# Performance work log

Hardware: AMD Instinct MI355X
Metric: run time of the kernel (lower is better)

The kernel has to match this reference:

```python
import jax, jax.numpy as jnp
import numpy as np
import math

B, T, D, H, L = 8, 1024, 128, 8, 2
DH = D // H            # head dim = 16
F = 2 * D              # ffn hidden = 256 (FFN_EXPANSION=2)
SCALE = math.sqrt(DH)  # sqrt of Q last dim per head


def layernorm(x, g, b):
    m = jnp.mean(x, axis=-1, keepdims=True)
    v = jnp.var(x, axis=-1, keepdims=True)
    return (x - m) * jax.lax.rsqrt(v + 1e-5) * g + b


def setup_inputs() -> dict:
    key = jax.random.key(0)
    ks = jax.random.split(key, 16)
    s = 1.0 / math.sqrt(D)
    r = lambda i, shp: jax.random.normal(ks[i], shp, dtype=jnp.float32) * s
    return {
        "x": jax.random.normal(ks[0], (B, T, D), dtype=jnp.float32),
        "y": jax.random.normal(ks[1], (B, T, D), dtype=jnp.float32),
        # shared qkv projections (no bias), per layer
        "Wq": r(2, (L, D, D)), "Wk": r(3, (L, D, D)), "Wv": r(4, (L, D, D)),
        "Wox": r(5, (L, D, D)), "box": jnp.zeros((L, D), jnp.float32),
        "Woy": r(6, (L, D, D)), "boy": jnp.zeros((L, D), jnp.float32),
        "ln1x_g": jnp.ones((L, D), jnp.float32), "ln1x_b": jnp.zeros((L, D), jnp.float32),
        "ln1y_g": jnp.ones((L, D), jnp.float32), "ln1y_b": jnp.zeros((L, D), jnp.float32),
        "ln2x_g": jnp.ones((L, D), jnp.float32), "ln2x_b": jnp.zeros((L, D), jnp.float32),
        "ln2y_g": jnp.ones((L, D), jnp.float32), "ln2y_b": jnp.zeros((L, D), jnp.float32),
        "fx_w1": r(7, (L, D, F)), "fx_b1": jnp.zeros((L, F), jnp.float32),
        "fx_w2": r(8, (L, F, D)), "fx_b2": jnp.zeros((L, D), jnp.float32),
        "fy_w1": r(9, (L, D, F)), "fy_b1": jnp.zeros((L, F), jnp.float32),
        "fy_w2": r(10, (L, F, D)), "fy_b2": jnp.zeros((L, D), jnp.float32),
    }


def _heads(t):
    # (B,T,D) -> (B,T,H,DH)
    return t.reshape(B, T, H, DH)


def _block(x, y, Wq, Wk, Wv, Wox, box, Woy, boy,
           ln1x_g, ln1x_b, ln1y_g, ln1y_b, ln2x_g, ln2x_b, ln2y_g, ln2y_b,
           fx_w1, fx_b1, fx_w2, fx_b2, fy_w1, fy_b1, fy_w2, fy_b2):
    xn = layernorm(x, ln1x_g, ln1x_b)
    yn = layernorm(y, ln1y_g, ln1y_b)
    # x-branch: Q from y, K/V from x ; y-branch: Q from x, K/V from y
    qx = _heads(yn @ Wq); kx = _heads(xn @ Wk); vx = _heads(xn @ Wv)
    qy = _heads(xn @ Wq); ky = _heads(yn @ Wk); vy = _heads(yn @ Wv)
    ax = jnp.einsum('bthd,bshd->bhts', qx, kx)  # (B,H,T,T)
    ay = jnp.einsum('bthd,bshd->bhts', qy, ky)
    # cat over heads + reshape(B,2,H,T,T) + mean(dim=1) == per-head average
    w = jax.nn.softmax((ax + ay) * (0.5 / SCALE), axis=-1)
    o1 = jnp.einsum('bhts,bshd->bthd', w, vx).reshape(B, T, D) @ Wox + box
    o2 = jnp.einsum('bhts,bshd->bthd', w, vy).reshape(B, T, D) @ Woy + boy
    x = x + o1
    y = y + o2
    xn2 = layernorm(x, ln2x_g, ln2x_b)
    yn2 = layernorm(y, ln2y_g, ln2y_b)
    x = x + jax.nn.gelu(xn2 @ fx_w1 + fx_b1, approximate=False) @ fx_w2 + fx_b2
    y = y + jax.nn.gelu(yn2 @ fy_w1 + fy_b1, approximate=False) @ fy_w2 + fy_b2
    return x, y


def reference(x, y, Wq, Wk, Wv, Wox, box, Woy, boy,
              ln1x_g, ln1x_b, ln1y_g, ln1y_b, ln2x_g, ln2x_b, ln2y_g, ln2y_b,
              fx_w1, fx_b1, fx_w2, fx_b2, fy_w1, fy_b1, fy_w2, fy_b2):
    for i in range(L):
        x, y = _block(x, y, Wq[i], Wk[i], Wv[i], Wox[i], box[i], Woy[i], boy[i],
                      ln1x_g[i], ln1x_b[i], ln1y_g[i], ln1y_b[i],
                      ln2x_g[i], ln2x_b[i], ln2y_g[i], ln2y_b[i],
                      fx_w1[i], fx_b1[i], fx_w2[i], fx_b2[i],
                      fy_w1[i], fy_b1[i], fy_w2[i], fy_b2[i])
    return (x, y)
```

## Files before the change

kernel.cpp:

```cpp
#include <hip/hip_runtime.h>
#include <cstddef>

#define BB   8
#define TT   1024
#define DDIM 128
#define HH   8
#define DHH  16
#define FF   256
#define BT   (BB * TT)

typedef unsigned short u16;
typedef __attribute__((ext_vector_type(8))) short short8;
typedef __attribute__((ext_vector_type(4))) float f32x4;

__device__ __forceinline__ u16 bf(float x) {
  unsigned u = __builtin_bit_cast(unsigned, x);
  u += 0x7fffu + ((u >> 16) & 1u);
  return (u16)(u >> 16);
}
__device__ __forceinline__ u16 bft(float x) {
  return (u16)(__builtin_bit_cast(unsigned, x) >> 16);
}
__device__ __forceinline__ float gelu_f(float x) {
  const float t = x * (0.79788456f + 0.03567740814f * x * x);
  return x / (1.0f + __expf(-2.0f * t));
}

struct PrepP { const float* W; u16* Wt; int K; int N; };
struct PrepArgs { PrepP p[18]; };

__global__ __launch_bounds__(256) void prep_k(PrepArgs a) {
  const PrepP pp = a.p[blockIdx.z];
  const int n0 = blockIdx.x * 64, k0 = blockIdx.y * 64;
  if (n0 >= pp.N || k0 >= pp.K) return;
  __shared__ float tile[64][65];
  const int tid = threadIdx.x;
  #pragma unroll
  for (int t = tid; t < 1024; t += 256) {
    const int kk = t >> 4, nn4 = (t & 15) << 2;
    float4 v = *(const float4*)(pp.W + (size_t)(k0 + kk) * pp.N + n0 + nn4);
    tile[nn4 + 0][kk] = v.x; tile[nn4 + 1][kk] = v.y;
    tile[nn4 + 2][kk] = v.z; tile[nn4 + 3][kk] = v.w;
  }
  __syncthreads();
  #pragma unroll
  for (int t = tid; t < 1024; t += 256) {
    const int nn = t >> 4, kk4 = (t & 15) << 2;
    ushort4 o;
    o.x = bf(tile[nn][kk4 + 0]); o.y = bf(tile[nn][kk4 + 1]);
    o.z = bf(tile[nn][kk4 + 2]); o.w = bf(tile[nn][kk4 + 3]);
    *(ushort4*)(pp.Wt + (size_t)(n0 + nn) * pp.K + k0 + kk4) = o;
  }
}

__global__ __launch_bounds__(256) void ln0_k(const float* __restrict__ X,
                                             const float* __restrict__ Y,
                                             const float* __restrict__ gx,
                                             const float* __restrict__ bx,
                                             const float* __restrict__ gy,
                                             const float* __restrict__ by,
                                             u16* __restrict__ ox,
                                             u16* __restrict__ oy) {
  const int which = blockIdx.y;
  const float* in = which ? Y : X;
  const float* g  = which ? gy : gx;
  const float* b  = which ? by : bx;
  u16* out        = which ? oy : ox;
  const int row  = blockIdx.x * 4 + (threadIdx.x >> 6);
  const int lane = threadIdx.x & 63;

  float2 v = *(const float2*)(in + (size_t)row * DDIM + lane * 2);
  float s  = v.x + v.y;
  float sq = v.x * v.x + v.y * v.y;
  #pragma unroll
  for (int off = 32; off >= 1; off >>= 1) {
    s  += __shfl_xor(s, off);
    sq += __shfl_xor(sq, off);
  }
  const float mean = s * (1.0f / DDIM);
  const float var  = sq * (1.0f / DDIM) - mean * mean;
  const float r    = rsqrtf(var + 1e-5f);
  float2 gg = *(const float2*)(g + lane * 2);
  float2 bb = *(const float2*)(b + lane * 2);
  ushort2 o;
  o.x = bf((v.x - mean) * r * gg.x + bb.x);
  o.y = bf((v.y - mean) * r * gg.y + bb.y);
  *(ushort2*)(out + (size_t)row * DDIM + lane * 2) = o;
}

struct GemmP { const u16* A; const u16* Wt; const float* bias; const float* res;
               float* outF; u16* outB; const float* g; const float* b; };
struct GemmArgs { GemmP p[6]; int ln; };

__global__ __launch_bounds__(256) void gemmf_k(GemmArgs a) {
  const GemmP pp = a.p[blockIdx.z];
  const int m0 = blockIdx.y * 32;
  __shared__ __align__(16) u16 As[32][136];
  __shared__ __align__(16) u16 Bs[128][136];
  __shared__ float2 stats[32][2];
  const int tid  = threadIdx.x;
  const int w    = tid >> 6;
  const int lane = tid & 63;
  const int l15  = lane & 15;
  const int quad = lane >> 4;
  const int wr = w & 1, wc = w >> 1;

  f32x4 acc[4];
  #pragma unroll
  for (int j = 0; j < 4; ++j) acc[j] = {0.f, 0.f, 0.f, 0.f};

  #pragma unroll
  for (int t = tid; t < 512; t += 256) {
    const int r = t >> 4, g8 = (t & 15) << 3;
    *(short8*)&As[r][g8] = *(const short8*)(pp.A + (size_t)(m0 + r) * 128 + g8);
  }
  #pragma unroll
  for (int t = tid; t < 2048; t += 256) {
    const int r = t >> 4, g8 = (t & 15) << 3;
    *(short8*)&Bs[r][g8] = *(const short8*)(pp.Wt + (size_t)r * 128 + g8);
  }
  __syncthreads();
  #pragma unroll
  for (int ks = 0; ks < 4; ++ks) {
    const short8 ar = *(const short8*)&As[wr * 16 + l15][ks * 32 + quad * 8];
    #pragma unroll
    for (int j = 0; j < 4; ++j) {
      const short8 br = *(const short8*)&Bs[wc * 64 + j * 16 + l15][ks * 32 + quad * 8];
      acc[j] = __builtin_amdgcn_mfma_f32_16x16x32_bf16(ar, br, acc[j], 0, 0, 0);
    }
  }

  #pragma unroll
  for (int j = 0; j < 4; ++j) {
    const int n = wc * 64 + j * 16 + l15;
    const float bias_v = pp.bias ? pp.bias[n] : 0.f;
    #pragma unroll
    for (int reg = 0; reg < 4; ++reg) {
      const int m = m0 + wr * 16 + quad * 4 + reg;
      float v = acc[j][reg] + bias_v;
      if (pp.res) v += pp.res[(size_t)m * 128 + n];
      acc[j][reg] = v;
      if (pp.outF) pp.outF[(size_t)m * 128 + n] = v;
    }
  }

  if (!a.ln) {
    #pragma unroll
    for (int j = 0; j < 4; ++j) {
      const int n = wc * 64 + j * 16 + l15;
      #pragma unroll
      for (int reg = 0; reg < 4; ++reg) {
        const int m = m0 + wr * 16 + quad * 4 + reg;
        pp.outB[(size_t)m * 128 + n] = bf(acc[j][reg]);
      }
    }
    return;
  }

  #pragma unroll
  for (int reg = 0; reg < 4; ++reg) {
    float s = 0.f, q = 0.f;
    #pragma unroll
    for (int j = 0; j < 4; ++j) { const float v = acc[j][reg]; s += v; q += v * v; }
    #pragma unroll
    for (int off = 8; off >= 1; off >>= 1) {
      s += __shfl_xor(s, off, 16);
      q += __shfl_xor(q, off, 16);
    }
    if (l15 == 0) stats[wr * 16 + quad * 4 + reg][wc] = make_float2(s, q);
  }
  __syncthreads();
  #pragma unroll
  for (int reg = 0; reg < 4; ++reg) {
    const int mloc = wr * 16 + quad * 4 + reg;
    const float2 s0 = stats[mloc][0], s1 = stats[mloc][1];
    const float mean = (s0.x + s1.x) * (1.0f / 128.f);
    const float var  = (s0.y + s1.y) * (1.0f / 128.f) - mean * mean;
    const float r    = rsqrtf(var + 1e-5f);
    #pragma unroll
    for (int j = 0; j < 4; ++j) {
      const int n = wc * 64 + j * 16 + l15;
      pp.outB[(size_t)(m0 + mloc) * 128 + n] =
          bf((acc[j][reg] - mean) * r * pp.g[n] + pp.b[n]);
    }
  }
}

struct FfnP { const u16* A; const u16* W1t; const float* b1;
              const u16* W2t; const float* b2; const float* res;
              float* outF; u16* outB; const float* g; const float* b; };
struct FfnArgs { FfnP p[2]; int ln; };

__global__ __launch_bounds__(256) void ffn_k(FfnArgs a) {
  const FfnP pp = a.p[blockIdx.y];
  const int m0 = blockIdx.x * 32;
  __shared__ __align__(16) u16 As[32][136];
  __shared__ __align__(16) u16 Bs[128][136];
  __shared__ __align__(16) u16 Hs[32][264];
  __shared__ float2 stats[32][2];
  const int tid  = threadIdx.x;
  const int w    = tid >> 6;
  const int lane = tid & 63;
  const int l15  = lane & 15;
  const int quad = lane >> 4;
  const int wr = w & 1, wc = w >> 1;

  #pragma unroll
  for (int t = tid; t < 512; t += 256) {
    const int r = t >> 4, g8 = (t & 15) << 3;
    *(short8*)&As[r][g8] = *(const short8*)(pp.A + (size_t)(m0 + r) * 128 + g8);
  }

  for (int nh = 0; nh < 2; ++nh) {
    #pragma unroll
    for (int t = tid; t < 2048; t += 256) {
      const int r = t >> 4, g8 = (t & 15) << 3;
      *(short8*)&Bs[r][g8] = *(const short8*)(pp.W1t + (size_t)(nh * 128 + r) * 128 + g8);
    }
    __syncthreads();
    f32x4 acc[4];
    #pragma unroll
    for (int j = 0; j < 4; ++j) acc[j] = {0.f, 0.f, 0.f, 0.f};
    #pragma unroll
    for (int ks = 0; ks < 4; ++ks) {
      const short8 ar = *(const short8*)&As[wr * 16 + l15][ks * 32 + quad * 8];
      #pragma unroll
      for (int j = 0; j < 4; ++j) {
        const short8 br = *(const short8*)&Bs[wc * 64 + j * 16 + l15][ks * 32 + quad * 8];
        acc[j] = __builtin_amdgcn_mfma_f32_16x16x32_bf16(ar, br, acc[j], 0, 0, 0);
      }
    }
    #pragma unroll
    for (int j = 0; j < 4; ++j) {
      const int n = wc * 64 + j * 16 + l15;
      const float bias_v = pp.b1[nh * 128 + n];
      #pragma unroll
      for (int reg = 0; reg < 4; ++reg) {
        const int mloc = wr * 16 + quad * 4 + reg;
        Hs[mloc][nh * 128 + n] = bf(gelu_f(acc[j][reg] + bias_v));
      }
    }
    __syncthreads();
  }

  f32x4 acc2[4];
  #pragma unroll
  for (int j = 0; j < 4; ++j) acc2[j] = {0.f, 0.f, 0.f, 0.f};
  for (int kh = 0; kh < 2; ++kh) {
    #pragma unroll
    for (int t = tid; t < 2048; t += 256) {
      const int r = t >> 4, g8 = (t & 15) << 3;
      *(short8*)&Bs[r][g8] = *(const short8*)(pp.W2t + (size_t)r * 256 + kh * 128 + g8);
    }
    __syncthreads();
    #pragma unroll
    for (int ks = 0; ks < 4; ++ks) {
      const short8 ar = *(const short8*)&Hs[wr * 16 + l15][kh * 128 + ks * 32 + quad * 8];
      #pragma unroll
      for (int j = 0; j < 4; ++j) {
        const short8 br = *(const short8*)&Bs[wc * 64 + j * 16 + l15][ks * 32 + quad * 8];
        acc2[j] = __builtin_amdgcn_mfma_f32_16x16x32_bf16(ar, br, acc2[j], 0, 0, 0);
      }
    }
    __syncthreads();
  }

  #pragma unroll
  for (int j = 0; j < 4; ++j) {
    const int n = wc * 64 + j * 16 + l15;
    const float bias_v = pp.b2[n];
    #pragma unroll
    for (int reg = 0; reg < 4; ++reg) {
      const int m = m0 + wr * 16 + quad * 4 + reg;
      float v = acc2[j][reg] + bias_v + pp.res[(size_t)m * 128 + n];
      acc2[j][reg] = v;
      pp.outF[(size_t)m * 128 + n] = v;
    }
  }
  if (!a.ln) return;
  #pragma unroll
  for (int reg = 0; reg < 4; ++reg) {
    float s = 0.f, q = 0.f;
    #pragma unroll
    for (int j = 0; j < 4; ++j) { const float v = acc2[j][reg]; s += v; q += v * v; }
    #pragma unroll
    for (int off = 8; off >= 1; off >>= 1) {
      s += __shfl_xor(s, off, 16);
      q += __shfl_xor(q, off, 16);
    }
    if (l15 == 0) stats[wr * 16 + quad * 4 + reg][wc] = make_float2(s, q);
  }
  __syncthreads();
  #pragma unroll
  for (int reg = 0; reg < 4; ++reg) {
    const int mloc = wr * 16 + quad * 4 + reg;
    const float2 s0 = stats[mloc][0], s1 = stats[mloc][1];
    const float mean = (s0.x + s1.x) * (1.0f / 128.f);
    const float var  = (s0.y + s1.y) * (1.0f / 128.f) - mean * mean;
    const float r    = rsqrtf(var + 1e-5f);
    #pragma unroll
    for (int j = 0; j < 4; ++j) {
      const int n = wc * 64 + j * 16 + l15;
      pp.outB[(size_t)(m0 + mloc) * 128 + n] =
          bf((acc2[j][reg] - mean) * r * pp.g[n] + pp.b[n]);
    }
  }
}

__global__ __launch_bounds__(256) void attn_k(const u16* __restrict__ qx,
                                              const u16* __restrict__ kx,
                                              const u16* __restrict__ vx,
                                              const u16* __restrict__ qy,
                                              const u16* __restrict__ ky,
                                              const u16* __restrict__ vy,
                                              u16* __restrict__ o1,
                                              u16* __restrict__ o2) {
  const int t0 = blockIdx.x * 64;
  const int bh = blockIdx.y;
  const int b = bh >> 3, h = bh & 7;
  const size_t base = (size_t)b * TT * DDIM + h * DHH;

  __shared__ __align__(16) u16 Ks[2][128][40];
  __shared__ __align__(16) u16 Vt[2][32][136];
  __shared__ __align__(16) u16 Ps[64][136];

  const int tid  = threadIdx.x;
  const int w    = tid >> 6;
  const int lane = tid & 63;
  const int l15  = lane & 15;
  const int quad = lane >> 4;

  const u16* qp = (quad < 2) ? qx : qy;
  const int dq = (quad & 1) * 8;
  const short8 qa = *(const short8*)(qp + base + (size_t)(t0 + w * 16 + l15) * DDIM + dq);

  f32x4 Of0 = {0.f, 0.f, 0.f, 0.f};
  f32x4 Of1 = {0.f, 0.f, 0.f, 0.f};
  float l_i[4] = {0.f, 0.f, 0.f, 0.f};

  const int ks_s = tid >> 2, ks_c = tid & 3;
  const u16* ks_p = (ks_c < 2) ? kx : ky;
  const int ks_d8 = (ks_c & 1) * 8;
  const int ks_col = (ks_c < 2 ? 0 : 16) + ks_d8;

  const u16* vs_p = (w < 2) ? vx : vy;
  const int vs_cc = (w & 1) * 8;
  const int vs_cb = (w < 2 ? 0 : 16) + vs_cc;

  #define STAGE(kt, buf)                                                          \
    do {                                                                          \
      const int s0_ = (kt) * 128;                                                 \
      _Pragma("unroll")                                                           \
      for (int p = 0; p < 2; ++p) {                                               \
        const int s = ks_s + p * 64;                                              \
        *(short8*)&Ks[buf][s][ks_col] =                                           \
            *(const short8*)(ks_p + base + (size_t)(s0_ + s) * DDIM + ks_d8);     \
      }                                                                           \
      _Pragma("unroll")                                                           \
      for (int p = 0; p < 2; ++p) {                                               \
        const int sl = lane + p * 64;                                             \
        const short8 v8 =                                                         \
            *(const short8*)(vs_p + base + (size_t)(s0_ + sl) * DDIM + vs_cc);    \
        _Pragma("unroll")                                                         \
        for (int e = 0; e < 8; ++e) Vt[buf][vs_cb + e][sl] = (u16)v8[e];          \
      }                                                                           \
    } while (0)

  STAGE(0, 0);

  for (int kt = 0; kt < TT / 128; ++kt) {
    const int buf = kt & 1;
    __syncthreads();
    if (kt + 1 < TT / 128) STAGE(kt + 1, buf ^ 1);

    f32x4 Sf[8];
    #pragma unroll
    for (int t = 0; t < 8; ++t) {
      short8 kb = *(const short8*)&Ks[buf][t * 16 + l15][quad * 8];
      f32x4 z = {0.f, 0.f, 0.f, 0.f};
      Sf[t] = __builtin_amdgcn_mfma_f32_16x16x32_bf16(qa, kb, z, 0, 0, 0);
    }

    #pragma unroll
    for (int reg = 0; reg < 4; ++reg) {
      const int q = w * 16 + quad * 4 + reg;
      float sum = 0.f;
      #pragma unroll
      for (int t = 0; t < 8; ++t) {
        const float p = exp2f(Sf[t][reg] * 0.18033688011112042f);
        sum += p;
        Ps[q][t * 16 + l15] = bft(p);
      }
      l_i[reg] += sum;
    }

    #pragma unroll
    for (int sh = 0; sh < 4; ++sh) {
      short8 pa  = *(const short8*)&Ps[w * 16 + l15][sh * 32 + quad * 8];
      short8 vb0 = *(const short8*)&Vt[buf][l15][sh * 32 + quad * 8];
      short8 vb1 = *(const short8*)&Vt[buf][16 + l15][sh * 32 + quad * 8];
      Of0 = __builtin_amdgcn_mfma_f32_16x16x32_bf16(pa, vb0, Of0, 0, 0, 0);
      Of1 = __builtin_amdgcn_mfma_f32_16x16x32_bf16(pa, vb1, Of1, 0, 0, 0);
    }
  }
  #undef STAGE

  #pragma unroll
  for (int reg = 0; reg < 4; ++reg) {
    float l = l_i[reg];
    #pragma unroll
    for (int off = 8; off >= 1; off >>= 1) l += __shfl_xor(l, off, 16);
    const float inv = 1.0f / l;
    const size_t r = base + (size_t)(t0 + w * 16 + quad * 4 + reg) * DDIM + l15;
    o1[r] = bf(Of0[reg] * inv);
    o2[r] = bf(Of1[reg] * inv);
  }
}

extern "C" void kernel_launch(void* const* d_in, const int* in_sizes, int n_in,
                              void* d_out, int out_size, void* d_ws, size_t ws_size,
                              hipStream_t stream) {
  const float* x_in  = (const float*)d_in[0];
  const float* y_in  = (const float*)d_in[1];
  const float* Wq    = (const float*)d_in[2];
  const float* Wk    = (const float*)d_in[3];
  const float* Wv    = (const float*)d_in[4];
  const float* Wox   = (const float*)d_in[5];
  const float* box   = (const float*)d_in[6];
  const float* Woy   = (const float*)d_in[7];
  const float* boy   = (const float*)d_in[8];
  const float* ln1xg = (const float*)d_in[9];
  const float* ln1xb = (const float*)d_in[10];
  const float* ln1yg = (const float*)d_in[11];
  const float* ln1yb = (const float*)d_in[12];
  const float* ln2xg = (const float*)d_in[13];
  const float* ln2xb = (const float*)d_in[14];
  const float* ln2yg = (const float*)d_in[15];
  const float* ln2yb = (const float*)d_in[16];
  const float* fxw1  = (const float*)d_in[17];
  const float* fxb1  = (const float*)d_in[18];
  const float* fxw2  = (const float*)d_in[19];
  const float* fxb2  = (const float*)d_in[20];
  const float* fyw1  = (const float*)d_in[21];
  const float* fyb1  = (const float*)d_in[22];
  const float* fyw2  = (const float*)d_in[23];
  const float* fyb2  = (const float*)d_in[24];

  const size_t S = (size_t)BT * DDIM;
  float* X = (float*)d_out;
  float* Y = X + S;

  char* wsb = (char*)d_ws;
  auto carve = [&](size_t bytes) { char* p = wsb; wsb += (bytes + 255) & ~(size_t)255; return p; };
  u16* xn  = (u16*)carve(S * 2);
  u16* yn  = (u16*)carve(S * 2);
  u16* qx  = (u16*)carve(S * 2);
  u16* kx  = (u16*)carve(S * 2);
  u16* vx  = (u16*)carve(S * 2);
  u16* qy  = (u16*)carve(S * 2);
  u16* ky  = (u16*)carve(S * 2);
  u16* vy  = (u16*)carve(S * 2);
  u16* ob1 = (u16*)carve(S * 2);
  u16* ob2 = (u16*)carve(S * 2);
  u16* WqT[2], *WkT[2], *WvT[2], *WoxT[2], *WoyT[2];
  u16* f1xT[2], *f1yT[2], *f2xT[2], *f2yT[2];
  for (int l = 0; l < 2; ++l) {
    WqT[l]  = (u16*)carve(16384 * 2);
    WkT[l]  = (u16*)carve(16384 * 2);
    WvT[l]  = (u16*)carve(16384 * 2);
    WoxT[l] = (u16*)carve(16384 * 2);
    WoyT[l] = (u16*)carve(16384 * 2);
    f1xT[l] = (u16*)carve(32768 * 2);
    f1yT[l] = (u16*)carve(32768 * 2);
    f2xT[l] = (u16*)carve(32768 * 2);
    f2yT[l] = (u16*)carve(32768 * 2);
  }

  {
    PrepArgs a;
    int idx = 0;
    for (int l = 0; l < 2; ++l) {
      a.p[idx++] = {Wq  + (size_t)l * 16384, WqT[l],  128, 128};
      a.p[idx++] = {Wk  + (size_t)l * 16384, WkT[l],  128, 128};
      a.p[idx++] = {Wv  + (size_t)l * 16384, WvT[l],  128, 128};
      a.p[idx++] = {Wox + (size_t)l * 16384, WoxT[l], 128, 128};
      a.p[idx++] = {Woy + (size_t)l * 16384, WoyT[l], 128, 128};
      a.p[idx++] = {fxw1 + (size_t)l * 32768, f1xT[l], 128, 256};
      a.p[idx++] = {fyw1 + (size_t)l * 32768, f1yT[l], 128, 256};
      a.p[idx++] = {fxw2 + (size_t)l * 32768, f2xT[l], 256, 128};
      a.p[idx++] = {fyw2 + (size_t)l * 32768, f2yT[l], 256, 128};
    }
    prep_k<<<dim3(4, 4, 18), 256, 0, stream>>>(a);
  }

  ln0_k<<<dim3(BT / 4, 2), 256, 0, stream>>>(x_in, y_in, ln1xg, ln1xb, ln1yg, ln1yb, xn, yn);

  for (int l = 0; l < 2; ++l) {
    const size_t bo  = (size_t)l * DDIM;
    const size_t fbo = (size_t)l * FF;

    {
      GemmArgs a = {}; a.ln = 0;
      a.p[0] = {yn, WqT[l], nullptr, nullptr, nullptr, qx, nullptr, nullptr};
      a.p[1] = {xn, WkT[l], nullptr, nullptr, nullptr, kx, nullptr, nullptr};
      a.p[2] = {xn, WvT[l], nullptr, nullptr, nullptr, vx, nullptr, nullptr};
      a.p[3] = {xn, WqT[l], nullptr, nullptr, nullptr, qy, nullptr, nullptr};
      a.p[4] = {yn, WkT[l], nullptr, nullptr, nullptr, ky, nullptr, nullptr};
      a.p[5] = {yn, WvT[l], nullptr, nullptr, nullptr, vy, nullptr, nullptr};
      gemmf_k<<<dim3(1, BT / 32, 6), 256, 0, stream>>>(a);
    }
    attn_k<<<dim3(TT / 64, BB * HH), 256, 0, stream>>>(qx, kx, vx, qy, ky, vy, ob1, ob2);
    {
      const float* resx = (l == 0) ? x_in : X;
      const float* resy = (l == 0) ? y_in : Y;
      GemmArgs a = {}; a.ln = 1;
      a.p[0] = {ob1, WoxT[l], box + bo, resx, X, xn, ln2xg + bo, ln2xb + bo};
      a.p[1] = {ob2, WoyT[l], boy + bo, resy, Y, yn, ln2yg + bo, ln2yb + bo};
      gemmf_k<<<dim3(1, BT / 32, 2), 256, 0, stream>>>(a);
    }
    {
      FfnArgs a = {}; a.ln = (l == 0) ? 1 : 0;
      if (l == 0) {
        a.p[0] = {xn, f1xT[l], fxb1 + fbo, f2xT[l], fxb2 + bo, X, X, xn,
                  ln1xg + DDIM, ln1xb + DDIM};
        a.p[1] = {yn, f1yT[l], fyb1 + fbo, f2yT[l], fyb2 + bo, Y, Y, yn,
                  ln1yg + DDIM, ln1yb + DDIM};
      } else {
        a.p[0] = {xn, f1xT[l], fxb1 + fbo, f2xT[l], fxb2 + bo, X, X, nullptr,
                  nullptr, nullptr};
        a.p[1] = {yn, f1yT[l], fyb1 + fbo, f2yT[l], fyb2 + bo, Y, Y, nullptr,
                  nullptr, nullptr};
      }
      ffn_k<<<dim3(BT / 32, 2), 256, 0, stream>>>(a);
    }
  }
}
```

Measured before the change: 270.9 us.

## Write V pre-transposed from projection GEMM and shrink attention key tiles

The QKV projection GEMM now writes V directly in a head-major transposed layout (b,h,d,s), so the attention kernel can stage V with vectorized short8 loads instead of scattering elements into a transposed shared tile. The attention kernel also switches to 64-key tiles with smaller shared buffers, and swaps the MFMA operand order so each lane holds scores for one query row. That allows packed ushort4 stores of P and a single row-sum reduction per lane. The trade-off is twice as many loop iterations and barriers per block, plus strided 8-byte transposed stores in the GEMM epilogue.

```diff
diff --git a/kernel.cpp b/kernel.cpp
--- a/kernel.cpp
+++ b/kernel.cpp
@@ -89,7 +89,7 @@
 }
 
 struct GemmP { const u16* A; const u16* Wt; const float* bias; const float* res;
-               float* outF; u16* outB; const float* g; const float* b; };
+               float* outF; u16* outB; const float* g; const float* b; u16* outT; };
 struct GemmArgs { GemmP p[6]; int ln; };
 
 __global__ __launch_bounds__(256) void gemmf_k(GemmArgs a) {
@@ -130,6 +130,21 @@
     }
   }
 
+  if (pp.outT) {
+    const int m_base = m0 + wr * 16 + quad * 4;
+    const int bb_ = m_base >> 10, s = m_base & 1023;
+    #pragma unroll
+    for (int j = 0; j < 4; ++j) {
+      const int n = wc * 64 + j * 16 + l15;
+      const int h = n >> 4, c = n & 15;
+      ushort4 o;
+      o.x = bf(acc[j][0]); o.y = bf(acc[j][1]);
+      o.z = bf(acc[j][2]); o.w = bf(acc[j][3]);
+      *(ushort4*)(pp.outT + (((size_t)(bb_ * 8 + h) * 16 + c) << 10) + s) = o;
+    }
+    return;
+  }
+
   #pragma unroll
   for (int j = 0; j < 4; ++j) {
     const int n = wc * 64 + j * 16 + l15;
@@ -145,13 +160,15 @@
   }
 
   if (!a.ln) {
-    #pragma unroll
-    for (int j = 0; j < 4; ++j) {
-      const int n = wc * 64 + j * 16 + l15;
+    if (pp.outB) {
       #pragma unroll
-      for (int reg = 0; reg < 4; ++reg) {
-        const int m = m0 + wr * 16 + quad * 4 + reg;
-        pp.outB[(size_t)m * 128 + n] = bf(acc[j][reg]);
+      for (int j = 0; j < 4; ++j) {
+        const int n = wc * 64 + j * 16 + l15;
+        #pragma unroll
+        for (int reg = 0; reg < 4; ++reg) {
+          const int m = m0 + wr * 16 + quad * 4 + reg;
+          pp.outB[(size_t)m * 128 + n] = bf(acc[j][reg]);
+        }
       }
     }
     return;
@@ -309,10 +326,10 @@
 
 __global__ __launch_bounds__(256) void attn_k(const u16* __restrict__ qx,
                                               const u16* __restrict__ kx,
-                                              const u16* __restrict__ vx,
                                               const u16* __restrict__ qy,
                                               const u16* __restrict__ ky,
-                                              const u16* __restrict__ vy,
+                                              const u16* __restrict__ vtx,
+                                              const u16* __restrict__ vty,
                                               u16* __restrict__ o1,
                                               u16* __restrict__ o2) {
   const int t0 = blockIdx.x * 64;
@@ -320,9 +337,9 @@
   const int b = bh >> 3, h = bh & 7;
   const size_t base = (size_t)b * TT * DDIM + h * DHH;
 
-  __shared__ __align__(16) u16 Ks[2][128][40];
-  __shared__ __align__(16) u16 Vt[2][32][136];
-  __shared__ __align__(16) u16 Ps[64][136];
+  __shared__ __align__(16) u16 Ks[2][64][40];
+  __shared__ __align__(16) u16 Vt[2][32][72];
+  __shared__ __align__(16) u16 Ps[64][72];
 
   const int tid  = threadIdx.x;
   const int w    = tid >> 6;
@@ -336,66 +353,55 @@
 
   f32x4 Of0 = {0.f, 0.f, 0.f, 0.f};
   f32x4 Of1 = {0.f, 0.f, 0.f, 0.f};
-  float l_i[4] = {0.f, 0.f, 0.f, 0.f};
+  float l_i = 0.f;
 
   const int ks_s = tid >> 2, ks_c = tid & 3;
   const u16* ks_p = (ks_c < 2) ? kx : ky;
   const int ks_d8 = (ks_c & 1) * 8;
   const int ks_col = (ks_c < 2 ? 0 : 16) + ks_d8;
 
-  const u16* vs_p = (w < 2) ? vx : vy;
-  const int vs_cc = (w & 1) * 8;
-  const int vs_cb = (w < 2 ? 0 : 16) + vs_cc;
+  const int vs_c = tid >> 3;
+  const int vs_s8 = (tid & 7) * 8;
+  const u16* vs_row = (vs_c < 16) ? (vtx + (((size_t)bh * 16 + vs_c) << 10))
+                                  : (vty + (((size_t)bh * 16 + (vs_c - 16)) << 10));
 
   #define STAGE(kt, buf)                                                          \
     do {                                                                          \
-      const int s0_ = (kt) * 128;                                                 \
-      _Pragma("unroll")                                                           \
-      for (int p = 0; p < 2; ++p) {                                               \
-        const int s = ks_s + p * 64;                                              \
-        *(short8*)&Ks[buf][s][ks_col] =                                           \
-            *(const short8*)(ks_p + base + (size_t)(s0_ + s) * DDIM + ks_d8);     \
-      }                                                                           \
-      _Pragma("unroll")                                                           \
-      for (int p = 0; p < 2; ++p) {                                               \
-        const int sl = lane + p * 64;                                             \
-        const short8 v8 =                                                         \
-            *(const short8*)(vs_p + base + (size_t)(s0_ + sl) * DDIM + vs_cc);    \
-        _Pragma("unroll")                                                         \
-        for (int e = 0; e < 8; ++e) Vt[buf][vs_cb + e][sl] = (u16)v8[e];          \
-      }                                                                           \
+      const int s0_ = (kt) * 64;                                                  \
+      *(short8*)&Ks[buf][ks_s][ks_col] =                                          \
+          *(const short8*)(ks_p + base + (size_t)(s0_ + ks_s) * DDIM + ks_d8);    \
+      *(short8*)&Vt[buf][vs_c][vs_s8] = *(const short8*)(vs_row + s0_ + vs_s8);   \
     } while (0)
 
   STAGE(0, 0);
 
-  for (int kt = 0; kt < TT / 128; ++kt) {
+  for (int kt = 0; kt < TT / 64; ++kt) {
     const int buf = kt & 1;
     __syncthreads();
-    if (kt + 1 < TT / 128) STAGE(kt + 1, buf ^ 1);
-
-    f32x4 Sf[8];
-    #pragma unroll
-    for (int t = 0; t < 8; ++t) {
+    if (kt + 1 < TT / 64) STAGE(kt + 1, buf ^ 1);
+
+    f32x4 Sf[4];
+    #pragma unroll
+    for (int t = 0; t < 4; ++t) {
       short8 kb = *(const short8*)&Ks[buf][t * 16 + l15][quad * 8];
       f32x4 z = {0.f, 0.f, 0.f, 0.f};
-      Sf[t] = __builtin_amdgcn_mfma_f32_16x16x32_bf16(qa, kb, z, 0, 0, 0);
-    }
-
-    #pragma unroll
-    for (int reg = 0; reg < 4; ++reg) {
-      const int q = w * 16 + quad * 4 + reg;
-      float sum = 0.f;
-      #pragma unroll
-      for (int t = 0; t < 8; ++t) {
-        const float p = exp2f(Sf[t][reg] * 0.18033688011112042f);
-        sum += p;
-        Ps[q][t * 16 + l15] = bft(p);
-      }
-      l_i[reg] += sum;
-    }
-
-    #pragma unroll
-    for (int sh = 0; sh < 4; ++sh) {
+      Sf[t] = __builtin_amdgcn_mfma_f32_16x16x32_bf16(kb, qa, z, 0, 0, 0);
+    }
+
+    #pragma unroll
+    for (int t = 0; t < 4; ++t) {
+      const float p0 = exp2f(Sf[t][0] * 0.18033688011112042f);
+      const float p1 = exp2f(Sf[t][1] * 0.18033688011112042f);
+      const float p2 = exp2f(Sf[t][2] * 0.18033688011112042f);
+      const float p3 = exp2f(Sf[t][3] * 0.18033688011112042f);
+      l_i += p0 + p1 + p2 + p3;
+      ushort4 pk;
+      pk.x = bft(p0); pk.y = bft(p1); pk.z = bft(p2); pk.w = bft(p3);
+      *(ushort4*)&Ps[w * 16 + l15][t * 16 + quad * 4] = pk;
+    }
+
+    #pragma unroll
+    for (int sh = 0; sh < 2; ++sh) {
       short8 pa  = *(const short8*)&Ps[w * 16 + l15][sh * 32 + quad * 8];
       short8 vb0 = *(const short8*)&Vt[buf][l15][sh * 32 + quad * 8];
       short8 vb1 = *(const short8*)&Vt[buf][16 + l15][sh * 32 + quad * 8];
@@ -405,12 +411,12 @@
   }
   #undef STAGE
 
+  l_i += __shfl_xor(l_i, 16);
+  l_i += __shfl_xor(l_i, 32);
   #pragma unroll
   for (int reg = 0; reg < 4; ++reg) {
-    float l = l_i[reg];
-    #pragma unroll
-    for (int off = 8; off >= 1; off >>= 1) l += __shfl_xor(l, off, 16);
-    const float inv = 1.0f / l;
+    const float lq = __shfl(l_i, quad * 4 + reg, 16);
+    const float inv = 1.0f / lq;
     const size_t r = base + (size_t)(t0 + w * 16 + quad * 4 + reg) * DDIM + l15;
     o1[r] = bf(Of0[reg] * inv);
     o2[r] = bf(Of1[reg] * inv);
@@ -456,10 +462,10 @@
   u16* yn  = (u16*)carve(S * 2);
   u16* qx  = (u16*)carve(S * 2);
   u16* kx  = (u16*)carve(S * 2);
-  u16* vx  = (u16*)carve(S * 2);
   u16* qy  = (u16*)carve(S * 2);
   u16* ky  = (u16*)carve(S * 2);
-  u16* vy  = (u16*)carve(S * 2);
+  u16* vxT = (u16*)carve(S * 2);
+  u16* vyT = (u16*)carve(S * 2);
   u16* ob1 = (u16*)carve(S * 2);
   u16* ob2 = (u16*)carve(S * 2);
   u16* WqT[2], *WkT[2], *WvT[2], *WoxT[2], *WoyT[2];
@@ -501,21 +507,21 @@
 
     {
       GemmArgs a = {}; a.ln = 0;
-      a.p[0] = {yn, WqT[l], nullptr, nullptr, nullptr, qx, nullptr, nullptr};
-      a.p[1] = {xn, WkT[l], nullptr, nullptr, nullptr, kx, nullptr, nullptr};
-      a.p[2] = {xn, WvT[l], nullptr, nullptr, nullptr, vx, nullptr, nullptr};
-      a.p[3] = {xn, WqT[l], nullptr, nullptr, nullptr, qy, nullptr, nullptr};
-      a.p[4] = {yn, WkT[l], nullptr, nullptr, nullptr, ky, nullptr, nullptr};
-      a.p[5] = {yn, WvT[l], nullptr, nullptr, nullptr, vy, nullptr, nullptr};
+      a.p[0] = {yn, WqT[l], nullptr, nullptr, nullptr, qx, nullptr, nullptr, nullptr};
+      a.p[1] = {xn, WkT[l], nullptr, nullptr, nullptr, kx, nullptr, nullptr, nullptr};
+      a.p[2] = {xn, WvT[l], nullptr, nullptr, nullptr, nullptr, nullptr, nullptr, vxT};
+      a.p[3] = {xn, WqT[l], nullptr, nullptr, nullptr, qy, nullptr, nullptr, nullptr};
+      a.p[4] = {yn, WkT[l], nullptr, nullptr, nullptr, ky, nullptr, nullptr, nullptr};
+      a.p[5] = {yn, WvT[l], nullptr, nullptr, nullptr, nullptr, nullptr, nullptr, vyT};
       gemmf_k<<<dim3(1, BT / 32, 6), 256, 0, stream>>>(a);
     }
-    attn_k<<<dim3(TT / 64, BB * HH), 256, 0, stream>>>(qx, kx, vx, qy, ky, vy, ob1, ob2);
+    attn_k<<<dim3(TT / 64, BB * HH), 256, 0, stream>>>(qx, kx, qy, ky, vxT, vyT, ob1, ob2);
     {
       const float* resx = (l == 0) ? x_in : X;
       const float* resy = (l == 0) ? y_in : Y;
       GemmArgs a = {}; a.ln = 1;
-      a.p[0] = {ob1, WoxT[l], box + bo, resx, X, xn, ln2xg + bo, ln2xb + bo};
-      a.p[1] = {ob2, WoyT[l], boy + bo, resy, Y, yn, ln2yg + bo, ln2yb + bo};
+      a.p[0] = {ob1, WoxT[l], box + bo, resx, X, xn, ln2xg + bo, ln2xb + bo, nullptr};
+      a.p[1] = {ob2, WoyT[l], boy + bo, resy, Y, yn, ln2yg + bo, ln2yb + bo, nullptr};
       gemmf_k<<<dim3(1, BT / 32, 2), 256, 0, stream>>>(a);
     }
     {
```

After: 251.5 us. -7.1%, faster.
